# Performance work log

Measured on AMD Instinct MI355X. Metric: run time of the kernel, lower is better.

## Reference

```python
import jax, jax.numpy as jnp
import numpy as np

D_MODEL = 512; N_HEADS = 8; D_HIDDEN = 512
STACK_DEPTH = 48; STACK_WIDTH = 128; D_FF = 2048; D_SS = 128
SEQ = 512; BATCH = 16
EP = 1e-4; MAX_ITER = 100


def nonsat(x):
    # fixed-point iteration y_ = (2y^3/3 + x)/(y^2+1); torch detaches y each step,
    # so grads flow only through x in the final step. Loop runs on stopped values.
    xs = jax.lax.stop_gradient(x)
    step = lambda y: (2.0 * y ** 3 / 3.0 + xs) / (y * y + 1.0)
    def cond(s):
        y, y_, i = s
        return jnp.logical_and(jnp.mean(jnp.abs(y_ - y)) > EP, i <= MAX_ITER)
    def body(s):
        y, y_, i = s
        return (y_, step(y_), i + 1)
    y_last, _, _ = jax.lax.while_loop(cond, body, (xs, step(xs), jnp.int32(0)))
    return (2.0 * y_last ** 3 / 3.0 + x) / (y_last * y_last + 1.0)


def layer_norm(x, g, b, eps=1e-5):
    m = jnp.mean(x, axis=-1, keepdims=True)
    v = jnp.mean((x - m) ** 2, axis=-1, keepdims=True)
    return (x - m) / jnp.sqrt(v + eps) * g + b


def mha(x, k_mask, wi, bi, wo, bo):
    # x: (S,B,E), torch nn.MultiheadAttention with combined in_proj, causal mask
    S, B, E = x.shape
    H = N_HEADS; hd = E // H
    qkv = x @ wi.T + bi
    q, k, v = jnp.split(qkv, 3, axis=-1)
    to_heads = lambda t: t.reshape(S, B, H, hd).transpose(1, 2, 0, 3)  # (B,H,S,hd)
    q = to_heads(q) * (hd ** -0.5)
    k = to_heads(k); v = to_heads(v)
    scores = jnp.einsum('bhqd,bhkd->bhqk', q, k)
    causal = jnp.triu(jnp.full((S, S), -jnp.inf, dtype=x.dtype), 1)
    scores = scores + causal
    scores = jnp.where(k_mask[:, None, None, :], -jnp.inf, scores)
    a = jax.nn.softmax(scores, axis=-1)
    o = jnp.einsum('bhqk,bhkd->bhqd', a, v).transpose(2, 0, 1, 3).reshape(S, B, E)
    return o @ wo.T + bo


def setup_inputs() -> dict:
    key = jax.random.key(0)
    ks = iter(jax.random.split(key, 32))
    E = D_MODEL
    def w(shape, fan_in):
        return (jax.random.normal(next(ks), shape, jnp.float32) / np.sqrt(fan_in)).astype(jnp.float32)
    inp = {
        'x_in': jax.random.normal(next(ks), (SEQ, BATCH, E), jnp.float32),
        'hidden_prev': jax.random.normal(next(ks), (BATCH, SEQ, D_HIDDEN), jnp.float32),
        'stack_prev': jax.random.normal(next(ks), (BATCH, SEQ, STACK_DEPTH, STACK_WIDTH), jnp.float32),
        'k_mask': jnp.zeros((BATCH, SEQ), dtype=bool),
        'in_proj_w': w((3 * E, E), E), 'in_proj_b': jnp.zeros((3 * E,), jnp.float32),
        'out_proj_w': w((E, E), E), 'out_proj_b': jnp.zeros((E,), jnp.float32),
        'ln1_g': jnp.ones((E,), jnp.float32), 'ln1_b': jnp.zeros((E,), jnp.float32),
        'ln2_g': jnp.ones((E,), jnp.float32), 'ln2_b': jnp.zeros((E,), jnp.float32),
        'ff_w1': w((D_FF, E), E), 'ff_b1': jnp.zeros((D_FF,), jnp.float32),
        'ff_w2': w((E, D_FF), D_FF), 'ff_b2': jnp.zeros((E,), jnp.float32),
        'W_w': w((D_HIDDEN, E), E), 'W_b': jnp.zeros((D_HIDDEN,), jnp.float32),
        'R_w': w((D_HIDDEN, D_HIDDEN), D_HIDDEN), 'R_b': jnp.zeros((D_HIDDEN,), jnp.float32),
        'P_w': w((D_HIDDEN, STACK_WIDTH), STACK_WIDTH), 'P_b': jnp.zeros((D_HIDDEN,), jnp.float32),
        'V_w': w((D_SS, E + D_HIDDEN), E + D_HIDDEN),
        'U_w': w((E, D_SS), D_SS),
        'A_w': w((3, D_HIDDEN), D_HIDDEN), 'A_b': jnp.zeros((3,), jnp.float32),
        'D_w': w((STACK_WIDTH, D_HIDDEN), D_HIDDEN), 'D_b': jnp.zeros((STACK_WIDTH,), jnp.float32),
    }
    return inp


def reference(x_in, hidden_prev, stack_prev, k_mask,
              in_proj_w, in_proj_b, out_proj_w, out_proj_b,
              ln1_g, ln1_b, ln2_g, ln2_b,
              ff_w1, ff_b1, ff_w2, ff_b2,
              W_w, W_b, R_w, R_b, P_w, P_b,
              V_w, U_w, A_w, A_b, D_w, D_b):
    # sublayer 1: pre-norm residual multihead self-attention
    x = x_in + mha(layer_norm(x_in, ln1_g, ln1_b), k_mask,
                   in_proj_w, in_proj_b, out_proj_w, out_proj_b)
    # stack-augmented memory update
    stack_x = stack_prev[:, :, 0, :]                       # (B,S,W) stack top
    xb = x.transpose(1, 0, 2)                              # (B,S,E)
    hidden = xb @ W_w.T + W_b + hidden_prev @ R_w.T + R_b + stack_x @ P_w.T + P_b
    hidden = nonsat(hidden)                                # (B,S,Dh)
    vx = jnp.concatenate([x, hidden.transpose(1, 0, 2)], axis=-1)  # (S,B,E+Dh)
    y = jax.nn.softmax(vx @ V_w.T, axis=-1) @ U_w.T        # (S,B,E)
    x = 0.5 * (x + y)
    stack_inp = nonsat(hidden @ D_w.T + D_b)[:, :, None, :]        # (B,S,1,W)
    controls = jax.nn.softmax(hidden @ A_w.T + A_b, axis=-1)       # (B,S,3)
    a_push = controls[:, :, 0, None, None]
    a_pop = controls[:, :, 1, None, None]
    a_noop = controls[:, :, 2, None, None]
    zeros_bot = jnp.zeros_like(stack_prev[:, :, :1])
    stack_down = jnp.concatenate([stack_prev[:, :, 1:], zeros_bot], axis=2)
    stack_up = jnp.concatenate([stack_inp, stack_prev[:, :, :-1]], axis=2)
    stack = a_noop * stack_prev + a_push * stack_up + a_pop * stack_down
    # sublayer 2: pre-norm residual position-wise FFN
    h = layer_norm(x, ln2_g, ln2_b)
    x = x + (jax.nn.relu(h @ ff_w1.T + ff_b1) @ ff_w2.T + ff_b2)
    return (x, hidden, stack)
```

## Files before the change

### kernel.cpp

```cpp
#include <hip/hip_runtime.h>
#include <stdint.h>

typedef unsigned short u16;
typedef short short8 __attribute__((ext_vector_type(8)));
typedef float f32x4 __attribute__((ext_vector_type(4)));

__device__ __forceinline__ u16 f2b(float f) {
    uint32_t x = __float_as_uint(f);
    uint32_t r = x + 0x7fffu + ((x >> 16) & 1u);
    return (u16)(r >> 16);
}

__device__ __forceinline__ float nonsat_f(float x) {
    float y = x;
#pragma unroll
    for (int t = 0; t < 14; ++t) {
        const float y2 = y * y;
        y = (0.66666667f * y2 * y + x) / (y2 + 1.f);
    }
    return y;
}

__device__ __forceinline__ void gl2lds16(const u16* g, u16* l) {
    __builtin_amdgcn_global_load_lds(
        (const __attribute__((address_space(1))) unsigned int*)g,
        (__attribute__((address_space(3))) unsigned int*)l, 16, 0, 0);
}

template <int MT, int MODE, bool RELU>
__global__ __launch_bounds__(256) void gemm_k(
    const u16* __restrict__ A, int lda,
    const u16* __restrict__ B, int ldb,
    const float* __restrict__ bias,
    int M, int N, int K,
    u16* __restrict__ out_b, float* __restrict__ out_f,
    const float* __restrict__ res_f, u16* __restrict__ out_b2)
{
    constexpr int MI = MT / 64;
    constexpr int WI = MT / 32;
    const int tn = blockIdx.x, tm = blockIdx.y;
    const int tid = threadIdx.x;
    const int wave = tid >> 6, lane = tid & 63;
    const int quad = lane >> 4, mm = lane & 15;
    const int wr = (wave >> 1) * (MT / 2), wc = (wave & 1) * 64;

    __shared__ __align__(16) u16 As[MT * 32];
    __shared__ __align__(16) u16 Bs[128 * 32];

    const f32x4 vzero = {0.f, 0.f, 0.f, 0.f};
    f32x4 acc[WI][4];
#pragma unroll
    for (int i = 0; i < WI; i++)
#pragma unroll
        for (int j = 0; j < 4; j++) acc[i][j] = vzero;

    const int lr = tid >> 2;
    const int lc = (tid & 3) * 8;
    const u16* ag[MI];
#pragma unroll
    for (int h = 0; h < MI; h++)
        ag[h] = A + (size_t)(tm * MT + lr + h * 64) * lda + lc;
    const u16* bg0 = B + (size_t)(tn * 128 + lr) * ldb + lc;
    const u16* bg1 = B + (size_t)(tn * 128 + lr + 64) * ldb + lc;
    u16* asl[MI];
#pragma unroll
    for (int h = 0; h < MI; h++) asl[h] = As + h * 2048 + wave * 512;
    u16* bsl0 = Bs + wave * 512;
    u16* bsl1 = Bs + 2048 + wave * 512;

    for (int kt = 0; kt < K; kt += 32) {
        __syncthreads();
#pragma unroll
        for (int h = 0; h < MI; h++) gl2lds16(ag[h] + kt, asl[h]);
        gl2lds16(bg0 + kt, bsl0);
        gl2lds16(bg1 + kt, bsl1);
        asm volatile("s_waitcnt vmcnt(0)" ::: "memory");
        __syncthreads();
        short8 af[WI], bfr[4];
#pragma unroll
        for (int i = 0; i < WI; i++) af[i] = *(const short8*)(As + (wr + i * 16 + mm) * 32 + quad * 8);
#pragma unroll
        for (int j = 0; j < 4; j++) bfr[j] = *(const short8*)(Bs + (wc + j * 16 + mm) * 32 + quad * 8);
#pragma unroll
        for (int i = 0; i < WI; i++)
#pragma unroll
            for (int j = 0; j < 4; j++)
                acc[i][j] = __builtin_amdgcn_mfma_f32_16x16x32_bf16(af[i], bfr[j], acc[i][j], 0, 0, 0);
    }

    if constexpr (MODE == 8) {
        __shared__ __align__(16) float Sm[64 * 130];
#pragma unroll
        for (int j = 0; j < 4; j++)
#pragma unroll
            for (int i = 0; i < WI; i++)
#pragma unroll
                for (int r = 0; r < 4; r++)
                    Sm[(wr + i * 16 + quad * 4 + r) * 130 + wc + j * 16 + mm] = acc[i][j][r];
        __syncthreads();
#pragma unroll
        for (int rr = 0; rr < 16; ++rr) {
            const int row_l = wave * 16 + rr;
            const float a = Sm[row_l * 130 + lane];
            const float b = Sm[row_l * 130 + 64 + lane];
            float mx = fmaxf(a, b);
#pragma unroll
            for (int off = 1; off < 64; off <<= 1) mx = fmaxf(mx, __shfl_xor(mx, off));
            const float ea = __expf(a - mx), eb = __expf(b - mx);
            float s = ea + eb;
#pragma unroll
            for (int off = 1; off < 64; off <<= 1) s += __shfl_xor(s, off);
            const float inv = 1.f / s;
            const size_t rowg = (size_t)tm * MT + row_l;
            out_b[rowg * 128 + lane] = f2b(ea * inv);
            out_b[rowg * 128 + 64 + lane] = f2b(eb * inv);
        }
        return;
    }

#pragma unroll
    for (int j = 0; j < 4; j++) {
        const int colg = tn * 128 + wc + j * 16 + mm;
        const float bv = bias ? bias[colg] : 0.f;
#pragma unroll
        for (int i = 0; i < WI; i++) {
#pragma unroll
            for (int r = 0; r < 4; r++) {
                const int rowg = tm * MT + wr + i * 16 + quad * 4 + r;
                float v = acc[i][j][r] + bv;
                const size_t off = (size_t)rowg * N + colg;
                if constexpr (MODE == 0) {
                    if (RELU) v = fmaxf(v, 0.f);
                    out_b[off] = f2b(v);
                } else if constexpr (MODE == 3) {
                    v += res_f[off];
                    out_f[off] = v;
                    const u16 hb = f2b(v);
                    out_b[(size_t)rowg * 1024 + colg] = hb;
                    out_b2[((size_t)(rowg & 15) * 512 + (rowg >> 4)) * 1152 + colg] = hb;
                } else if constexpr (MODE == 4) {
                    v = 0.5f * (v + res_f[off]);
                    out_f[off] = v;
                } else if constexpr (MODE == 5) {
                    v += res_f[off];
                    out_f[off] = v;
                } else if constexpr (MODE == 6) {
                    v = nonsat_f(v);
                    out_f[off] = v;
                    out_b[((size_t)(rowg & 511) * 16 + (rowg >> 9)) * 1024 + 512 + colg] = f2b(v);
                } else {
                    v = nonsat_f(v);
                    out_f[off] = v;
                }
            }
        }
    }
}

struct CvtArgs {
    const float* s[12];
    unsigned cum[13];
};

static constexpr unsigned C_INPJ = 0;
static constexpr unsigned C_OUTP = 786432;
static constexpr unsigned C_FF1W = 1048576;
static constexpr unsigned C_FF2W = 2097152;
static constexpr unsigned C_WRP  = 3145728;
static constexpr unsigned C_VW   = 3735552;
static constexpr unsigned C_UW   = 3866624;
static constexpr unsigned C_DW   = 3932160;
static constexpr unsigned C_WTOT = 3997696;
static constexpr unsigned C_TOTAL = 9240576;

__global__ __launch_bounds__(256) void cvt_k(CvtArgs a, u16* __restrict__ wa, u16* __restrict__ ha,
                                             const float* __restrict__ Wb, const float* __restrict__ Rb,
                                             const float* __restrict__ Pb, float* __restrict__ bsum)
{
    if (blockIdx.x == gridDim.x - 1) {
        if (threadIdx.x < 128) {
            const int c = threadIdx.x * 4;
#pragma unroll
            for (int k = 0; k < 4; k++) bsum[c + k] = Wb[c + k] + Rb[c + k] + Pb[c + k];
        }
        return;
    }
    const unsigned t = (blockIdx.x * 256u + threadIdx.x) * 8u;
    if (t >= a.cum[12]) return;
    int g = 0;
#pragma unroll
    for (int i = 1; i < 12; i++)
        if (t >= a.cum[i]) g = i;
    const unsigned e = t - a.cum[g];
    const float* src;
    u16* dst;
    if (g == 10) {
        src = a.s[10] + e;
        dst = ha + (size_t)(e >> 9) * 1152 + 512 + (e & 511);
    } else if (g == 11) {
        src = a.s[11] + (size_t)(e >> 7) * 6144 + (e & 127);
        dst = ha + (size_t)(e >> 7) * 1152 + 1024 + (e & 127);
    } else if (g == 4) {
        src = a.s[4] + e;
        dst = wa + C_WRP + (size_t)(e >> 9) * 1152 + (e & 511);
    } else if (g == 5) {
        src = a.s[5] + e;
        dst = wa + C_WRP + (size_t)(e >> 9) * 1152 + 512 + (e & 511);
    } else if (g == 6) {
        src = a.s[6] + e;
        dst = wa + C_WRP + (size_t)(e >> 7) * 1152 + 1024 + (e & 127);
    } else {
        src = a.s[g] + e;
        dst = wa + t;
    }
    float4 u0 = *(const float4*)src;
    float4 u1 = *(const float4*)(src + 4);
    __align__(16) u16 o[8] = {f2b(u0.x), f2b(u0.y), f2b(u0.z), f2b(u0.w),
                              f2b(u1.x), f2b(u1.y), f2b(u1.z), f2b(u1.w)};
    *(int4*)dst = *(const int4*)o;
}

__global__ __launch_bounds__(64) void attn_k(const u16* __restrict__ QKV, u16* __restrict__ O)
{
    const int qt = blockIdx.x;
    const int bh = blockIdx.y;
    const int b = bh >> 3, h = bh & 7;
    const int lane = threadIdx.x;
    const int quad = lane >> 4, mm = lane & 15;
    const int cbase = h * 64;
    const float NEGINF = -3.0e38f;

    __shared__ __align__(16) u16 Pl[64 * 72];
    __shared__ __align__(16) u16 Vl[64 * 72];

    short8 qf[4][2];
#pragma unroll
    for (int rt = 0; rt < 4; ++rt) {
        const int s = qt * 64 + rt * 16 + mm;
        const u16* p = QKV + ((size_t)s * 16 + b) * 1536 + cbase + quad * 8;
        qf[rt][0] = *(const short8*)(p);
        qf[rt][1] = *(const short8*)(p + 32);
    }

    const f32x4 vzero = {0.f, 0.f, 0.f, 0.f};
    f32x4 of[4][4];
#pragma unroll
    for (int i = 0; i < 4; i++)
#pragma unroll
        for (int j = 0; j < 4; j++) of[i][j] = vzero;
    float mrow[4][4], lrow[4][4];
#pragma unroll
    for (int i = 0; i < 4; i++)
#pragma unroll
        for (int r = 0; r < 4; r++) { mrow[i][r] = NEGINF; lrow[i][r] = 0.f; }

    for (int kt = 0; kt <= qt; ++kt) {
        short8 kf[4][2];
#pragma unroll
        for (int nt = 0; nt < 4; ++nt) {
            const int kk = kt * 64 + nt * 16 + mm;
            const u16* p = QKV + ((size_t)kk * 16 + b) * 1536 + 512 + cbase + quad * 8;
            kf[nt][0] = *(const short8*)(p);
            kf[nt][1] = *(const short8*)(p + 32);
        }
        f32x4 sf[4][4];
#pragma unroll
        for (int i = 0; i < 4; i++)
#pragma unroll
            for (int j = 0; j < 4; j++) sf[i][j] = vzero;
#pragma unroll
        for (int i = 0; i < 4; i++)
#pragma unroll
            for (int j = 0; j < 4; j++) {
                sf[i][j] = __builtin_amdgcn_mfma_f32_16x16x32_bf16(qf[i][0], kf[j][0], sf[i][j], 0, 0, 0);
                sf[i][j] = __builtin_amdgcn_mfma_f32_16x16x32_bf16(qf[i][1], kf[j][1], sf[i][j], 0, 0, 0);
            }
        {
            const int kk = lane >> 3, c8 = (lane & 7) * 8;
#pragma unroll
            for (int it = 0; it < 8; ++it) {
                const int key = kt * 64 + it * 8 + kk;
                int4 v = *(const int4*)(QKV + ((size_t)key * 16 + b) * 1536 + 1024 + cbase + c8);
                *(int4*)(Vl + (it * 8 + kk) * 72 + c8) = v;
            }
        }
        const bool diag = (kt == qt);
#pragma unroll
        for (int i = 0; i < 4; i++)
#pragma unroll
            for (int j = 0; j < 4; j++)
#pragma unroll
                for (int r = 0; r < 4; r++) {
                    float v = sf[i][j][r] * 0.125f;
                    if (diag) {
                        const int q = i * 16 + quad * 4 + r;
                        const int k = j * 16 + mm;
                        if (k > q) v = NEGINF;
                    }
                    sf[i][j][r] = v;
                }
#pragma unroll
        for (int i = 0; i < 4; i++) {
#pragma unroll
            for (int r = 0; r < 4; r++) {
                float mx = fmaxf(fmaxf(sf[i][0][r], sf[i][1][r]), fmaxf(sf[i][2][r], sf[i][3][r]));
                mx = fmaxf(mx, __shfl_xor(mx, 1));
                mx = fmaxf(mx, __shfl_xor(mx, 2));
                mx = fmaxf(mx, __shfl_xor(mx, 4));
                mx = fmaxf(mx, __shfl_xor(mx, 8));
                const float mnew = fmaxf(mrow[i][r], mx);
                const float alpha = __expf(mrow[i][r] - mnew);
                mrow[i][r] = mnew;
                float psum = 0.f;
#pragma unroll
                for (int j = 0; j < 4; j++) {
                    float p = __expf(sf[i][j][r] - mnew);
                    sf[i][j][r] = p;
                    psum += p;
                }
                psum += __shfl_xor(psum, 1);
                psum += __shfl_xor(psum, 2);
                psum += __shfl_xor(psum, 4);
                psum += __shfl_xor(psum, 8);
                lrow[i][r] = lrow[i][r] * alpha + psum;
#pragma unroll
                for (int j = 0; j < 4; j++) of[i][j][r] *= alpha;
            }
        }
#pragma unroll
        for (int i = 0; i < 4; i++)
#pragma unroll
            for (int j = 0; j < 4; j++)
#pragma unroll
                for (int r = 0; r < 4; r++)
                    Pl[(i * 16 + quad * 4 + r) * 72 + j * 16 + mm] = f2b(sf[i][j][r]);
        __syncthreads();
        short8 pa[4][2];
#pragma unroll
        for (int i = 0; i < 4; i++) {
            pa[i][0] = *(const short8*)(Pl + (i * 16 + mm) * 72 + quad * 8);
            pa[i][1] = *(const short8*)(Pl + (i * 16 + mm) * 72 + 32 + quad * 8);
        }
#pragma unroll
        for (int j = 0; j < 4; j++) {
#pragma unroll
            for (int kc = 0; kc < 2; ++kc) {
                short8 vb;
#pragma unroll
                for (int e = 0; e < 8; e++)
                    vb[e] = (short)Vl[(kc * 32 + quad * 8 + e) * 72 + j * 16 + mm];
#pragma unroll
                for (int i = 0; i < 4; i++)
                    of[i][j] = __builtin_amdgcn_mfma_f32_16x16x32_bf16(pa[i][kc], vb, of[i][j], 0, 0, 0);
            }
        }
        __syncthreads();
    }
#pragma unroll
    for (int i = 0; i < 4; i++)
#pragma unroll
        for (int r = 0; r < 4; r++) {
            const int s = qt * 64 + i * 16 + quad * 4 + r;
            const float inv = 1.f / lrow[i][r];
#pragma unroll
            for (int j = 0; j < 4; j++)
                O[((size_t)s * 16 + b) * 512 + cbase + j * 16 + mm] = f2b(of[i][j][r] * inv);
        }
}

__global__ __launch_bounds__(256) void ln_k(const float* __restrict__ x,
                                            const float* __restrict__ g,
                                            const float* __restrict__ be,
                                            u16* __restrict__ out)
{
    const int row = blockIdx.x * 4 + (threadIdx.x >> 6);
    const int lane = threadIdx.x & 63;
    const float* p = x + (size_t)row * 512 + lane * 8;
    float4 u0 = *(const float4*)p;
    float4 u1 = *(const float4*)(p + 4);
    float v[8] = {u0.x, u0.y, u0.z, u0.w, u1.x, u1.y, u1.z, u1.w};
    float s = 0.f, s2 = 0.f;
#pragma unroll
    for (int j = 0; j < 8; j++) { s += v[j]; s2 += v[j] * v[j]; }
#pragma unroll
    for (int off = 1; off < 64; off <<= 1) { s += __shfl_xor(s, off); s2 += __shfl_xor(s2, off); }
    const float mean = s * (1.f / 512.f);
    const float var = s2 * (1.f / 512.f) - mean * mean;
    const float rstd = rsqrtf(fmaxf(var, 0.f) + 1e-5f);
    float4 g0 = *(const float4*)(g + lane * 8);
    float4 g1 = *(const float4*)(g + lane * 8 + 4);
    float4 b0 = *(const float4*)(be + lane * 8);
    float4 b1 = *(const float4*)(be + lane * 8 + 4);
    const float gg[8] = {g0.x, g0.y, g0.z, g0.w, g1.x, g1.y, g1.z, g1.w};
    const float bb[8] = {b0.x, b0.y, b0.z, b0.w, b1.x, b1.y, b1.z, b1.w};
    __align__(16) u16 o[8];
#pragma unroll
    for (int j = 0; j < 8; j++)
        o[j] = f2b((v[j] - mean) * rstd * gg[j] + bb[j]);
    *(int4*)(out + (size_t)row * 512 + lane * 8) = *(const int4*)o;
}

__global__ __launch_bounds__(256) void controls_k(const float* __restrict__ H, const float* __restrict__ Aw,
                                                  const float* __restrict__ Ab, float* __restrict__ ctrl)
{
    const int row = blockIdx.x * 4 + (threadIdx.x >> 6);
    const int lane = threadIdx.x & 63;
    const float* hp = H + (size_t)row * 512 + lane * 8;
    float4 h0 = *(const float4*)hp;
    float4 h1 = *(const float4*)(hp + 4);
    const float hv[8] = {h0.x, h0.y, h0.z, h0.w, h1.x, h1.y, h1.z, h1.w};
    float d[3];
#pragma unroll
    for (int w = 0; w < 3; ++w) {
        const float* ap = Aw + w * 512 + lane * 8;
        float4 a0 = *(const float4*)ap;
        float4 a1 = *(const float4*)(ap + 4);
        const float av[8] = {a0.x, a0.y, a0.z, a0.w, a1.x, a1.y, a1.z, a1.w};
        float acc = 0.f;
#pragma unroll
        for (int j = 0; j < 8; j++) acc += hv[j] * av[j];
        d[w] = acc;
    }
#pragma unroll
    for (int off = 1; off < 64; off <<= 1) {
        d[0] += __shfl_xor(d[0], off);
        d[1] += __shfl_xor(d[1], off);
        d[2] += __shfl_xor(d[2], off);
    }
    const float l0 = d[0] + Ab[0], l1 = d[1] + Ab[1], l2 = d[2] + Ab[2];
    const float mx = fmaxf(l0, fmaxf(l1, l2));
    const float e0 = __expf(l0 - mx), e1 = __expf(l1 - mx), e2 = __expf(l2 - mx);
    const float inv = 1.f / (e0 + e1 + e2);
    if (lane == 0) {
        ctrl[(size_t)row * 3 + 0] = e0 * inv;
        ctrl[(size_t)row * 3 + 1] = e1 * inv;
        ctrl[(size_t)row * 3 + 2] = e2 * inv;
    }
}

__global__ __launch_bounds__(256) void stack_k(const float* __restrict__ sp_all, const float* __restrict__ sin,
                                               const float* __restrict__ ctrl, float* __restrict__ out)
{
    const int bs = blockIdx.x;
    const int t = blockIdx.y * 256 + threadIdx.x;
    const int d = t >> 4;
    const int w = (t & 15) * 8;
    const float* sp = sp_all + (size_t)bs * 6144;
    const float pu = ctrl[(size_t)bs * 3 + 0];
    const float po = ctrl[(size_t)bs * 3 + 1];
    const float no = ctrl[(size_t)bs * 3 + 2];
    float cur[8], up[8], dn[8];
    {
        const float* p = sp + d * 128 + w;
        float4 c0 = *(const float4*)p, c1 = *(const float4*)(p + 4);
        cur[0]=c0.x; cur[1]=c0.y; cur[2]=c0.z; cur[3]=c0.w; cur[4]=c1.x; cur[5]=c1.y; cur[6]=c1.z; cur[7]=c1.w;
    }
    {
        const int bb = bs >> 9, ss = bs & 511;
        const float* p = (d == 0) ? (sin + ((size_t)ss * 16 + bb) * 128 + w) : (sp + (d - 1) * 128 + w);
        float4 c0 = *(const float4*)p, c1 = *(const float4*)(p + 4);
        up[0]=c0.x; up[1]=c0.y; up[2]=c0.z; up[3]=c0.w; up[4]=c1.x; up[5]=c1.y; up[6]=c1.z; up[7]=c1.w;
    }
    if (d < 47) {
        const float* p = sp + (d + 1) * 128 + w;
        float4 c0 = *(const float4*)p, c1 = *(const float4*)(p + 4);
        dn[0]=c0.x; dn[1]=c0.y; dn[2]=c0.z; dn[3]=c0.w; dn[4]=c1.x; dn[5]=c1.y; dn[6]=c1.z; dn[7]=c1.w;
    } else {
#pragma unroll
        for (int j = 0; j < 8; j++) dn[j] = 0.f;
    }
    float o[8];
#pragma unroll
    for (int j = 0; j < 8; j++)
        o[j] = no * cur[j] + pu * up[j] + po * dn[j];
    float* q = out + (size_t)bs * 6144 + d * 128 + w;
    *(float4*)q = make_float4(o[0], o[1], o[2], o[3]);
    *(float4*)(q + 4) = make_float4(o[4], o[5], o[6], o[7]);
}

static constexpr size_t O_A1 = 0;
static constexpr size_t O_QKV = O_A1 + 8388608;
static constexpr size_t O_OATT = O_QKV + 25165824;
static constexpr size_t O_X1F = O_OATT + 8388608;
static constexpr size_t O_HPF = O_X1F + 16777216;
static constexpr size_t O_VL = O_HPF + 16777216;
static constexpr size_t O_X2F = O_VL + 4194304;
static constexpr size_t O_H2 = O_X2F + 16777216;
static constexpr size_t WS_NEED = O_H2 + 8388608;
static constexpr size_t O_VX = O_QKV;
static constexpr size_t O_PS = O_QKV + 16777216;
static constexpr size_t O_SIN = O_QKV + 18874368;
static constexpr size_t O_CTRL = O_QKV + 23068672;
static constexpr size_t O_FF1 = O_X1F;

static constexpr size_t WA_BYTES = (size_t)C_WTOT * 2;
static constexpr size_t HA_BYTES = (size_t)8192 * 1152 * 2;
static constexpr size_t STASH_BYTES = WA_BYTES + HA_BYTES;
static constexpr size_t STASH_OFF = 201326592 - STASH_BYTES;

extern "C" void kernel_launch(void* const* d_in, const int* in_sizes, int n_in,
                              void* d_out, int out_size, void* d_ws, size_t ws_size,
                              hipStream_t stream)
{
    (void)in_sizes; (void)n_in; (void)out_size;
    if (ws_size < WS_NEED) return;

    const float* x_in        = (const float*)d_in[0];
    const float* hidden_prev = (const float*)d_in[1];
    const float* stack_prev  = (const float*)d_in[2];
    const float* in_proj_w   = (const float*)d_in[4];
    const float* in_proj_b   = (const float*)d_in[5];
    const float* out_proj_w  = (const float*)d_in[6];
    const float* out_proj_b  = (const float*)d_in[7];
    const float* ln1_g       = (const float*)d_in[8];
    const float* ln1_b       = (const float*)d_in[9];
    const float* ln2_g       = (const float*)d_in[10];
    const float* ln2_b       = (const float*)d_in[11];
    const float* ff_w1       = (const float*)d_in[12];
    const float* ff_b1       = (const float*)d_in[13];
    const float* ff_w2       = (const float*)d_in[14];
    const float* ff_b2       = (const float*)d_in[15];
    const float* W_w         = (const float*)d_in[16];
    const float* W_b         = (const float*)d_in[17];
    const float* R_w         = (const float*)d_in[18];
    const float* R_b         = (const float*)d_in[19];
    const float* P_w         = (const float*)d_in[20];
    const float* P_b         = (const float*)d_in[21];
    const float* V_w         = (const float*)d_in[22];
    const float* U_w         = (const float*)d_in[23];
    const float* A_w         = (const float*)d_in[24];
    const float* A_b         = (const float*)d_in[25];
    const float* D_w         = (const float*)d_in[26];
    const float* D_b         = (const float*)d_in[27];

    char* ws = (char*)d_ws;
    u16* A1   = (u16*)(ws + O_A1);
    u16* QKV  = (u16*)(ws + O_QKV);
    u16* OATT = (u16*)(ws + O_OATT);
    float* X1F = (float*)(ws + O_X1F);
    float* bsum = (float*)(ws + O_VL);
    float* X2F = (float*)(ws + O_X2F);
    u16* H2   = (u16*)(ws + O_H2);
    u16* VX   = (u16*)(ws + O_VX);
    u16* PS   = (u16*)(ws + O_PS);
    float* SIN = (float*)(ws + O_SIN);
    float* CTRL = (float*)(ws + O_CTRL);
    u16* FF1  = (u16*)(ws + O_FF1);

    float* out = (float*)d_out;
    float* x_out = out;
    float* hid_out = out + 4194304;
    float* stack_out = out + 8388608;
    u16* wa = (u16*)((char*)stack_out + STASH_OFF);
    u16* ha = (u16*)((char*)wa + WA_BYTES);

    CvtArgs ca;
    ca.s[0] = in_proj_w; ca.s[1] = out_proj_w; ca.s[2] = ff_w1; ca.s[3] = ff_w2;
    ca.s[4] = W_w; ca.s[5] = R_w; ca.s[6] = P_w; ca.s[7] = V_w;
    ca.s[8] = U_w; ca.s[9] = D_w; ca.s[10] = hidden_prev; ca.s[11] = stack_prev;
    const unsigned cums[13] = {C_INPJ, C_OUTP, C_FF1W, C_FF2W, 3145728, 3407872, 3670016,
                               C_VW, C_UW, C_DW, C_WTOT, 8192000, C_TOTAL};
    for (int i = 0; i < 13; i++) ca.cum[i] = cums[i];
    cvt_k<<<4513, 256, 0, stream>>>(ca, wa, ha, W_b, R_b, P_b, bsum);

    ln_k<<<2048, 256, 0, stream>>>(x_in, ln1_g, ln1_b, A1);
    gemm_k<128, 0, false><<<dim3(12, 64), 256, 0, stream>>>(
        A1, 512, wa + C_INPJ, 512, in_proj_b, 8192, 1536, 512, QKV, nullptr, nullptr, nullptr);
    attn_k<<<dim3(8, 128), 64, 0, stream>>>(QKV, OATT);
    gemm_k<64, 3, false><<<dim3(4, 128), 256, 0, stream>>>(
        OATT, 512, wa + C_OUTP, 512, out_proj_b, 8192, 512, 512, VX, X1F, x_in, ha);
    gemm_k<64, 6, false><<<dim3(4, 128), 256, 0, stream>>>(
        ha, 1152, wa + C_WRP, 1152, bsum, 8192, 512, 1152, VX, hid_out, nullptr, nullptr);
    gemm_k<64, 8, false><<<dim3(1, 128), 256, 0, stream>>>(
        VX, 1024, wa + C_VW, 1024, nullptr, 8192, 128, 1024, PS, nullptr, nullptr, nullptr);
    gemm_k<64, 4, false><<<dim3(4, 128), 256, 0, stream>>>(
        PS, 128, wa + C_UW, 128, nullptr, 8192, 512, 128, nullptr, X2F, X1F, nullptr);
    gemm_k<64, 7, false><<<dim3(1, 128), 256, 0, stream>>>(
        VX + 512, 1024, wa + C_DW, 512, D_b, 8192, 128, 512, nullptr, SIN, nullptr, nullptr);
    controls_k<<<2048, 256, 0, stream>>>(hid_out, A_w, A_b, CTRL);
    ln_k<<<2048, 256, 0, stream>>>(X2F, ln2_g, ln2_b, H2);
    gemm_k<128, 0, true><<<dim3(16, 64), 256, 0, stream>>>(
        H2, 512, wa + C_FF1W, 512, ff_b1, 8192, 2048, 512, FF1, nullptr, nullptr, nullptr);
    gemm_k<64, 5, false><<<dim3(4, 128), 256, 0, stream>>>(
        FF1, 2048, wa + C_FF2W, 2048, ff_b2, 8192, 512, 2048, nullptr, x_out, X2F, nullptr);
    stack_k<<<dim3(8192, 3), 256, 0, stream>>>(stack_prev, SIN, CTRL, stack_out);
}
```

Before: 735.4 us.

## Double GEMM K-tile with XOR-swizzled LDS and fuse V/D projections into one launch

The GEMM kernel now loads 64-wide K slices per barrier instead of 32, halving the number of sync and wait rounds, and uses an XOR swizzle on LDS columns to avoid bank conflicts on fragment reads. The V and D projections are merged into one GEMM over a combined weight matrix, with D's weights zero-padded on the x half of the input. Column tile 0 does the softmax and tile 1 does the nonsat stack input, replacing two launches with one. This doubles LDS use per block, which may lower occupancy, and the zero padding spends extra MFMA work on the D half.

```diff
diff --git a/kernel.cpp b/kernel.cpp
--- a/kernel.cpp
+++ b/kernel.cpp
@@ -36,7 +36,7 @@
     u16* __restrict__ out_b, float* __restrict__ out_f,
     const float* __restrict__ res_f, u16* __restrict__ out_b2)
 {
-    constexpr int MI = MT / 64;
+    constexpr int AC = MT / 32;
     constexpr int WI = MT / 32;
     const int tn = blockIdx.x, tm = blockIdx.y;
     const int tid = threadIdx.x;
@@ -44,8 +44,8 @@
     const int quad = lane >> 4, mm = lane & 15;
     const int wr = (wave >> 1) * (MT / 2), wc = (wave & 1) * 64;
 
-    __shared__ __align__(16) u16 As[MT * 32];
-    __shared__ __align__(16) u16 Bs[128 * 32];
+    __shared__ __align__(16) u16 As[MT * 64];
+    __shared__ __align__(16) u16 Bs[128 * 64];
 
     const f32x4 vzero = {0.f, 0.f, 0.f, 0.f};
     f32x4 acc[WI][4];
@@ -54,66 +54,93 @@
 #pragma unroll
         for (int j = 0; j < 4; j++) acc[i][j] = vzero;
 
-    const int lr = tid >> 2;
-    const int lc = (tid & 3) * 8;
-    const u16* ag[MI];
-#pragma unroll
-    for (int h = 0; h < MI; h++)
-        ag[h] = A + (size_t)(tm * MT + lr + h * 64) * lda + lc;
-    const u16* bg0 = B + (size_t)(tn * 128 + lr) * ldb + lc;
-    const u16* bg1 = B + (size_t)(tn * 128 + lr + 64) * ldb + lc;
-    u16* asl[MI];
-#pragma unroll
-    for (int h = 0; h < MI; h++) asl[h] = As + h * 2048 + wave * 512;
-    u16* bsl0 = Bs + wave * 512;
-    u16* bsl1 = Bs + 2048 + wave * 512;
-
-    for (int kt = 0; kt < K; kt += 32) {
+    const int sr = wave * 8 + (lane >> 3);
+    const int sc = (((lane & 7) ^ (sr & 7))) * 8;
+
+    const u16* ag[AC];
+#pragma unroll
+    for (int h = 0; h < AC; h++)
+        ag[h] = A + (size_t)(tm * MT + h * 32 + sr) * lda + sc;
+    const u16* bg[4];
+#pragma unroll
+    for (int h = 0; h < 4; h++)
+        bg[h] = B + (size_t)(tn * 128 + h * 32 + sr) * ldb + sc;
+    u16* asl[AC];
+#pragma unroll
+    for (int h = 0; h < AC; h++) asl[h] = As + h * 2048 + wave * 512;
+    u16* bsl[4];
+#pragma unroll
+    for (int h = 0; h < 4; h++) bsl[h] = Bs + h * 2048 + wave * 512;
+
+    const int rx = mm & 7;
+
+    for (int kt = 0; kt < K; kt += 64) {
         __syncthreads();
 #pragma unroll
-        for (int h = 0; h < MI; h++) gl2lds16(ag[h] + kt, asl[h]);
-        gl2lds16(bg0 + kt, bsl0);
-        gl2lds16(bg1 + kt, bsl1);
+        for (int h = 0; h < AC; h++) gl2lds16(ag[h] + kt, asl[h]);
+#pragma unroll
+        for (int h = 0; h < 4; h++) gl2lds16(bg[h] + kt, bsl[h]);
         asm volatile("s_waitcnt vmcnt(0)" ::: "memory");
         __syncthreads();
-        short8 af[WI], bfr[4];
-#pragma unroll
-        for (int i = 0; i < WI; i++) af[i] = *(const short8*)(As + (wr + i * 16 + mm) * 32 + quad * 8);
-#pragma unroll
-        for (int j = 0; j < 4; j++) bfr[j] = *(const short8*)(Bs + (wc + j * 16 + mm) * 32 + quad * 8);
-#pragma unroll
-        for (int i = 0; i < WI; i++)
+#pragma unroll
+        for (int kk = 0; kk < 2; ++kk) {
+            const int gx = ((kk * 4 + quad) ^ rx) * 8;
+            short8 af[WI], bfr[4];
+#pragma unroll
+            for (int i = 0; i < WI; i++)
+                af[i] = *(const short8*)(As + (wr + i * 16 + mm) * 64 + gx);
 #pragma unroll
             for (int j = 0; j < 4; j++)
-                acc[i][j] = __builtin_amdgcn_mfma_f32_16x16x32_bf16(af[i], bfr[j], acc[i][j], 0, 0, 0);
-    }
-
-    if constexpr (MODE == 8) {
+                bfr[j] = *(const short8*)(Bs + (wc + j * 16 + mm) * 64 + gx);
+#pragma unroll
+            for (int i = 0; i < WI; i++)
+#pragma unroll
+                for (int j = 0; j < 4; j++)
+                    acc[i][j] = __builtin_amdgcn_mfma_f32_16x16x32_bf16(af[i], bfr[j], acc[i][j], 0, 0, 0);
+        }
+    }
+
+    if constexpr (MODE == 9) {
         __shared__ __align__(16) float Sm[64 * 130];
-#pragma unroll
-        for (int j = 0; j < 4; j++)
-#pragma unroll
-            for (int i = 0; i < WI; i++)
-#pragma unroll
-                for (int r = 0; r < 4; r++)
-                    Sm[(wr + i * 16 + quad * 4 + r) * 130 + wc + j * 16 + mm] = acc[i][j][r];
-        __syncthreads();
-#pragma unroll
-        for (int rr = 0; rr < 16; ++rr) {
-            const int row_l = wave * 16 + rr;
-            const float a = Sm[row_l * 130 + lane];
-            const float b = Sm[row_l * 130 + 64 + lane];
-            float mx = fmaxf(a, b);
-#pragma unroll
-            for (int off = 1; off < 64; off <<= 1) mx = fmaxf(mx, __shfl_xor(mx, off));
-            const float ea = __expf(a - mx), eb = __expf(b - mx);
-            float s = ea + eb;
-#pragma unroll
-            for (int off = 1; off < 64; off <<= 1) s += __shfl_xor(s, off);
-            const float inv = 1.f / s;
-            const size_t rowg = (size_t)tm * MT + row_l;
-            out_b[rowg * 128 + lane] = f2b(ea * inv);
-            out_b[rowg * 128 + 64 + lane] = f2b(eb * inv);
+        if (tn == 0) {
+#pragma unroll
+            for (int j = 0; j < 4; j++)
+#pragma unroll
+                for (int i = 0; i < WI; i++)
+#pragma unroll
+                    for (int r = 0; r < 4; r++)
+                        Sm[(wr + i * 16 + quad * 4 + r) * 130 + wc + j * 16 + mm] = acc[i][j][r];
+            __syncthreads();
+#pragma unroll
+            for (int rr = 0; rr < 16; ++rr) {
+                const int row_l = wave * 16 + rr;
+                const float a0 = Sm[row_l * 130 + lane];
+                const float a1 = Sm[row_l * 130 + 64 + lane];
+                float mx = fmaxf(a0, a1);
+#pragma unroll
+                for (int off = 1; off < 64; off <<= 1) mx = fmaxf(mx, __shfl_xor(mx, off));
+                const float ea = __expf(a0 - mx), eb = __expf(a1 - mx);
+                float s = ea + eb;
+#pragma unroll
+                for (int off = 1; off < 64; off <<= 1) s += __shfl_xor(s, off);
+                const float inv = 1.f / s;
+                const size_t rowg = (size_t)tm * MT + row_l;
+                out_b[rowg * 128 + lane] = f2b(ea * inv);
+                out_b[rowg * 128 + 64 + lane] = f2b(eb * inv);
+            }
+        } else {
+#pragma unroll
+            for (int j = 0; j < 4; j++) {
+                const int col_l = wc + j * 16 + mm;
+                const float bv = bias[col_l];
+#pragma unroll
+                for (int i = 0; i < WI; i++)
+#pragma unroll
+                    for (int r = 0; r < 4; r++) {
+                        const int rowg = tm * MT + wr + i * 16 + quad * 4 + r;
+                        out_f[(size_t)rowg * 128 + col_l] = nonsat_f(acc[i][j][r] + bv);
+                    }
+            }
         }
         return;
     }
@@ -144,13 +171,10 @@
                 } else if constexpr (MODE == 5) {
                     v += res_f[off];
                     out_f[off] = v;
-                } else if constexpr (MODE == 6) {
+                } else {
                     v = nonsat_f(v);
                     out_f[off] = v;
                     out_b[((size_t)(rowg & 511) * 16 + (rowg >> 9)) * 1024 + 512 + colg] = f2b(v);
-                } else {
-                    v = nonsat_f(v);
-                    out_f[off] = v;
                 }
             }
         }
@@ -158,8 +182,8 @@
 }
 
 struct CvtArgs {
-    const float* s[12];
-    unsigned cum[13];
+    const float* s[13];
+    unsigned cum[14];
 };
 
 static constexpr unsigned C_INPJ = 0;
@@ -167,11 +191,9 @@
 static constexpr unsigned C_FF1W = 1048576;
 static constexpr unsigned C_FF2W = 2097152;
 static constexpr unsigned C_WRP  = 3145728;
-static constexpr unsigned C_VW   = 3735552;
-static constexpr unsigned C_UW   = 3866624;
-static constexpr unsigned C_DW   = 3932160;
-static constexpr unsigned C_WTOT = 3997696;
-static constexpr unsigned C_TOTAL = 9240576;
+static constexpr unsigned C_VD   = 3735552;
+static constexpr unsigned C_UW   = 3997696;
+static constexpr unsigned C_WTOT = 4063232;
 
 __global__ __launch_bounds__(256) void cvt_k(CvtArgs a, u16* __restrict__ wa, u16* __restrict__ ha,
                                              const float* __restrict__ Wb, const float* __restrict__ Rb,
@@ -186,33 +208,29 @@
         return;
     }
     const unsigned t = (blockIdx.x * 256u + threadIdx.x) * 8u;
-    if (t >= a.cum[12]) return;
+    if (t >= a.cum[13]) return;
     int g = 0;
 #pragma unroll
-    for (int i = 1; i < 12; i++)
+    for (int i = 1; i < 13; i++)
         if (t >= a.cum[i]) g = i;
     const unsigned e = t - a.cum[g];
-    const float* src;
+    const float* src = nullptr;
     u16* dst;
-    if (g == 10) {
-        src = a.s[10] + e;
-        dst = ha + (size_t)(e >> 9) * 1152 + 512 + (e & 511);
-    } else if (g == 11) {
-        src = a.s[11] + (size_t)(e >> 7) * 6144 + (e & 127);
-        dst = ha + (size_t)(e >> 7) * 1152 + 1024 + (e & 127);
-    } else if (g == 4) {
-        src = a.s[4] + e;
-        dst = wa + C_WRP + (size_t)(e >> 9) * 1152 + (e & 511);
-    } else if (g == 5) {
-        src = a.s[5] + e;
-        dst = wa + C_WRP + (size_t)(e >> 9) * 1152 + 512 + (e & 511);
-    } else if (g == 6) {
-        src = a.s[6] + e;
-        dst = wa + C_WRP + (size_t)(e >> 7) * 1152 + 1024 + (e & 127);
-    } else {
-        src = a.s[g] + e;
-        dst = wa + t;
-    }
+    if (g <= 3) { src = a.s[g] + e; dst = wa + t; }
+    else if (g == 4) { src = a.s[4] + e; dst = wa + C_WRP + (size_t)(e >> 9) * 1152 + (e & 511); }
+    else if (g == 5) { src = a.s[5] + e; dst = wa + C_WRP + (size_t)(e >> 9) * 1152 + 512 + (e & 511); }
+    else if (g == 6) { src = a.s[6] + e; dst = wa + C_WRP + (size_t)(e >> 7) * 1152 + 1024 + (e & 127); }
+    else if (g == 7) { src = a.s[7] + e; dst = wa + C_VD + e; }
+    else if (g == 8) { src = a.s[8] + e; dst = wa + C_VD + 131072 + (size_t)(e >> 9) * 1024 + 512 + (e & 511); }
+    else if (g == 9) {
+        dst = wa + C_VD + 131072 + (size_t)(e >> 9) * 1024 + (e & 511);
+        int4 z = make_int4(0, 0, 0, 0);
+        *(int4*)dst = z;
+        return;
+    }
+    else if (g == 10) { src = a.s[10] + e; dst = wa + C_UW + e; }
+    else if (g == 11) { src = a.s[11] + e; dst = ha + (size_t)(e >> 9) * 1152 + 512 + (e & 511); }
+    else { src = a.s[12] + (size_t)(e >> 7) * 6144 + (e & 127); dst = ha + (size_t)(e >> 7) * 1152 + 1024 + (e & 127); }
     float4 u0 = *(const float4*)src;
     float4 u1 = *(const float4*)(src + 4);
     __align__(16) u16 o[8] = {f2b(u0.x), f2b(u0.y), f2b(u0.z), f2b(u0.w),
@@ -557,11 +575,12 @@
     CvtArgs ca;
     ca.s[0] = in_proj_w; ca.s[1] = out_proj_w; ca.s[2] = ff_w1; ca.s[3] = ff_w2;
     ca.s[4] = W_w; ca.s[5] = R_w; ca.s[6] = P_w; ca.s[7] = V_w;
-    ca.s[8] = U_w; ca.s[9] = D_w; ca.s[10] = hidden_prev; ca.s[11] = stack_prev;
-    const unsigned cums[13] = {C_INPJ, C_OUTP, C_FF1W, C_FF2W, 3145728, 3407872, 3670016,
-                               C_VW, C_UW, C_DW, C_WTOT, 8192000, C_TOTAL};
-    for (int i = 0; i < 13; i++) ca.cum[i] = cums[i];
-    cvt_k<<<4513, 256, 0, stream>>>(ca, wa, ha, W_b, R_b, P_b, bsum);
+    ca.s[8] = D_w; ca.s[9] = nullptr; ca.s[10] = U_w; ca.s[11] = hidden_prev;
+    ca.s[12] = stack_prev;
+    const unsigned cums[14] = {0, 786432, 1048576, 2097152, 3145728, 3407872, 3670016,
+                               3735552, 3866624, 3932160, 3997696, 4063232, 8257536, 9306112};
+    for (int i = 0; i < 14; i++) ca.cum[i] = cums[i];
+    cvt_k<<<4545, 256, 0, stream>>>(ca, wa, ha, W_b, R_b, P_b, bsum);
 
     ln_k<<<2048, 256, 0, stream>>>(x_in, ln1_g, ln1_b, A1);
     gemm_k<128, 0, false><<<dim3(12, 64), 256, 0, stream>>>(
@@ -571,12 +590,10 @@
         OATT, 512, wa + C_OUTP, 512, out_proj_b, 8192, 512, 512, VX, X1F, x_in, ha);
     gemm_k<64, 6, false><<<dim3(4, 128), 256, 0, stream>>>(
         ha, 1152, wa + C_WRP, 1152, bsum, 8192, 512, 1152, VX, hid_out, nullptr, nullptr);
-    gemm_k<64, 8, false><<<dim3(1, 128), 256, 0, stream>>>(
-        VX, 1024, wa + C_VW, 1024, nullptr, 8192, 128, 1024, PS, nullptr, nullptr, nullptr);
+    gemm_k<64, 9, false><<<dim3(2, 128), 256, 0, stream>>>(
+        VX, 1024, wa + C_VD, 1024, D_b, 8192, 256, 1024, PS, SIN, nullptr, nullptr);
     gemm_k<64, 4, false><<<dim3(4, 128), 256, 0, stream>>>(
         PS, 128, wa + C_UW, 128, nullptr, 8192, 512, 128, nullptr, X2F, X1F, nullptr);
-    gemm_k<64, 7, false><<<dim3(1, 128), 256, 0, stream>>>(
-        VX + 512, 1024, wa + C_DW, 512, D_b, 8192, 128, 512, nullptr, SIN, nullptr, nullptr);
     controls_k<<<2048, 256, 0, stream>>>(hid_out, A_w, A_b, CTRL);
     ln_k<<<2048, 256, 0, stream>>>(X2F, ln2_g, ln2_b, H2);
     gemm_k<128, 0, true><<<dim3(16, 64), 256, 0, stream>>>(
```

Result: slower. 958.2 us (+30.3%).
